# Performance work log

Measured on AMD Instinct MI355X. Metric: run time of the kernel, lower is better.

The kernel has to match this reference:

```python
import jax, jax.numpy as jnp
import numpy as np


def setup_inputs() -> dict:
    key = jax.random.key(0)
    k1, k2, k3 = jax.random.split(key, 3)
    N, M, D, K = 8192, 8192, 512, 128
    x = jax.random.normal(k1, (N, D), dtype=jnp.float32)
    target = jax.random.normal(k2, (M, D), dtype=jnp.float32)
    W = jax.random.normal(k3, (D, K), dtype=jnp.float32) * 0.05
    return {"x": x, "target": target, "W": W}


def reference(x, target, W):
    # phi_Brenier(x): convex potential f(x) = logsumexp(x @ W)  -> [N]
    phi_b = jax.nn.logsumexp(x @ W, axis=-1)
    # phi_Kantorovich = 0.5||x||^2 - phi_Brenier  -> [N]
    x_sq = jnp.sum(x * x, axis=-1)
    phi_k = 0.5 * x_sq - phi_b
    t_sq = jnp.sum(target * target, axis=-1)
    DD = 0.5 * (x_sq[:, None] + t_sq[None, :] - 2.0 * (x @ target.T))
    # C-transform: min over source points  -> [M]
    phi_c = jnp.min(DD - phi_k[:, None], axis=0)
    # Kantorovich dual objective (scalar)
    return jnp.mean(phi_k) + jnp.mean(phi_c)
```

## Files before the change

kernel.cpp:

```cpp
#include <hip/hip_runtime.h>
#include <hip/hip_bf16.h>
#include <stdint.h>

typedef __attribute__((ext_vector_type(8))) short short8;
typedef __attribute__((ext_vector_type(4))) float f32x4;
typedef __attribute__((ext_vector_type(16))) float f32x16;
typedef __attribute__((ext_vector_type(4))) int i32x4;
typedef __attribute__((ext_vector_type(8))) int i32x8;

#define N_PTS 8192
#define M_PTS 8192
#define DIM   512
#define KDIM  128

__device__ __forceinline__ unsigned fenc(float f) {
  unsigned u = __float_as_uint(f);
  return (u & 0x80000000u) ? ~u : (u | 0x80000000u);
}
__device__ __forceinline__ float fdec(unsigned k) {
  unsigned u = (k & 0x80000000u) ? (k ^ 0x80000000u) : ~k;
  return __uint_as_float(u);
}

__device__ __forceinline__ unsigned short f2bf(float f) {
  union { __hip_bfloat16 h; unsigned short u; } c;
  c.h = __float2bfloat16(f);
  return c.u;
}

__device__ __forceinline__ unsigned f2e4m3(float f) {
  unsigned u = __float_as_uint(f);
  unsigned s = (u >> 24) & 0x80;
  unsigned mag = u & 0x7fffffffu;
  unsigned r = mag + 0x0007ffffu + ((mag >> 20) & 1u);
  int e = (int)(r >> 23) - 127;
  if (e < -6) return s;
  unsigned m = (r >> 20) & 7u;
  return s | (unsigned)((e + 7) << 3) | m;
}

__device__ __forceinline__ void async_copy16(const void* g, void* l) {
  __builtin_amdgcn_global_load_lds(
      (const __attribute__((address_space(1))) void*)g,
      (__attribute__((address_space(3))) void*)l, 16, 0, 0);
}

__device__ __forceinline__ int swz_slot(int row, int slot) {
  return slot ^ ((row >> 1) & 3);
}

__device__ __forceinline__ int chunk_key(int row) {
  return ((row >> 1) & 3) ^ ((row >> 3) & 1) ^ (((row >> 4) & 1) << 1);
}

#define BARRIER __builtin_amdgcn_s_barrier()

__global__ __launch_bounds__(256)
void prep_all_kernel(const float* __restrict__ x, const float* __restrict__ tgt,
                     const float* __restrict__ W,
                     unsigned short* __restrict__ Xb, unsigned char* __restrict__ Xf8,
                     unsigned char* __restrict__ TfT, unsigned short* __restrict__ WbT,
                     float* __restrict__ xsq, float* __restrict__ tsq,
                     unsigned* __restrict__ keys) {
  const int bid = blockIdx.x;
  const int tid = threadIdx.x;
  if (bid >= (N_PTS + M_PTS) / 4) {
    const int o = (bid - (N_PTS + M_PTS) / 4) * 256 + tid;
    const int k = o >> 9, d = o & 511;
    WbT[o] = f2bf(W[d * KDIM + k]);
    return;
  }
  const int gw = (bid * 256 + tid) >> 6;
  const int j = tid & 63;
  float s;
  if (gw < N_PTS) {
    const float* src = x + (size_t)gw * DIM + j * 8;
    float4 v0 = *(const float4*)src;
    float4 v1 = *(const float4*)(src + 4);
    s = v0.x * v0.x + v0.y * v0.y + v0.z * v0.z + v0.w * v0.w +
        v1.x * v1.x + v1.y * v1.y + v1.z * v1.z + v1.w * v1.w;
    unsigned short* db = Xb + (size_t)gw * DIM + j * 8;
    ushort4 ob0, ob1;
    ob0.x = f2bf(v0.x); ob0.y = f2bf(v0.y); ob0.z = f2bf(v0.z); ob0.w = f2bf(v0.w);
    ob1.x = f2bf(v1.x); ob1.y = f2bf(v1.y); ob1.z = f2bf(v1.z); ob1.w = f2bf(v1.w);
    *(ushort4*)db = ob0;
    *(ushort4*)(db + 4) = ob1;
    unsigned long long p = (unsigned long long)f2e4m3(v0.x)
        | ((unsigned long long)f2e4m3(v0.y) << 8)
        | ((unsigned long long)f2e4m3(v0.z) << 16)
        | ((unsigned long long)f2e4m3(v0.w) << 24)
        | ((unsigned long long)f2e4m3(v1.x) << 32)
        | ((unsigned long long)f2e4m3(v1.y) << 40)
        | ((unsigned long long)f2e4m3(v1.z) << 48)
        | ((unsigned long long)f2e4m3(v1.w) << 56);
    *(unsigned long long*)(Xf8 + (size_t)gw * DIM + j * 8) = p;
#pragma unroll
    for (int m = 1; m <= 32; m <<= 1) s += __shfl_xor(s, m);
    if (j == 0) xsq[gw] = s;
  } else {
    const int tr = gw - N_PTS;
    const float* src = tgt + (size_t)tr * DIM + j * 8;
    float4 v0 = *(const float4*)src;
    float4 v1 = *(const float4*)(src + 4);
    s = v0.x * v0.x + v0.y * v0.y + v0.z * v0.z + v0.w * v0.w +
        v1.x * v1.x + v1.y * v1.y + v1.z * v1.z + v1.w * v1.w;
    unsigned long long p = (unsigned long long)f2e4m3(v0.x)
        | ((unsigned long long)f2e4m3(v0.y) << 8)
        | ((unsigned long long)f2e4m3(v0.z) << 16)
        | ((unsigned long long)f2e4m3(v0.w) << 24)
        | ((unsigned long long)f2e4m3(v1.x) << 32)
        | ((unsigned long long)f2e4m3(v1.y) << 40)
        | ((unsigned long long)f2e4m3(v1.z) << 48)
        | ((unsigned long long)f2e4m3(v1.w) << 56);
    *(unsigned long long*)(TfT + ((size_t)(j >> 3) * M_PTS + tr) * 64 + (j & 7) * 8) = p;
#pragma unroll
    for (int m = 1; m <= 32; m <<= 1) s += __shfl_xor(s, m);
    if (j == 0) { tsq[tr] = s; keys[tr] = 0xFFFFFFFFu; }
  }
}

__global__ __launch_bounds__(256)
void phi_b_kernel(const short* __restrict__ Xb, const short* __restrict__ WbT,
                  float* __restrict__ phi_b) {
  __shared__ __align__(16) short As[32 * 32];
  __shared__ __align__(16) short Bs[128 * 32];
  __shared__ __align__(16) float lg[32][136];

  const int tid = threadIdx.x;
  const int wave = tid >> 6, lane = tid & 63;
  const int n0 = blockIdx.x * 32;
  const int fr = lane & 15, g = lane >> 4;
  const int wc = wave;

  const int srow = tid >> 2;
  const int sk8 = swz_slot(srow, tid & 3) * 8;
  const int ra = tid >> 2;
  const int ska = swz_slot(ra, tid & 3) * 8;

  f32x4 acc[2][2] = {};
  for (int kt = 0; kt < 16; ++kt) {
    const int k0 = kt * 32;
    if (wave < 2)
      async_copy16(Xb + (size_t)(n0 + ra) * DIM + k0 + ska, &As[wave * 512]);
    async_copy16(WbT + (size_t)srow * DIM + k0 + sk8, &Bs[wave * 512]);
    async_copy16(WbT + (size_t)(srow + 64) * DIM + k0 + sk8, &Bs[2048 + wave * 512]);
    __syncthreads();
    short8 a[2], b[2];
#pragma unroll
    for (int i = 0; i < 2; ++i) {
      const int R = i * 16 + fr;
      a[i] = *(const short8*)&As[R * 32 + swz_slot(R, g) * 8];
    }
#pragma unroll
    for (int jx = 0; jx < 2; ++jx) {
      const int R = wc * 32 + jx * 16 + fr;
      b[jx] = *(const short8*)&Bs[R * 32 + swz_slot(R, g) * 8];
    }
#pragma unroll
    for (int i = 0; i < 2; ++i)
#pragma unroll
      for (int jx = 0; jx < 2; ++jx)
        acc[i][jx] = __builtin_amdgcn_mfma_f32_16x16x32_bf16(a[i], b[jx], acc[i][jx], 0, 0, 0);
    __syncthreads();
  }

  const int rq = g * 4;
#pragma unroll
  for (int i = 0; i < 2; ++i)
#pragma unroll
    for (int jx = 0; jx < 2; ++jx)
#pragma unroll
      for (int q = 0; q < 4; ++q)
        lg[i * 16 + rq + q][wc * 32 + jx * 16 + fr] = acc[i][jx][q];
  __syncthreads();

  const int row = tid >> 3, c8 = tid & 7;
  const float4* lr = (const float4*)(&lg[row][c8 * 16]);
  float mx = -3.4e38f;
#pragma unroll
  for (int c = 0; c < 4; ++c) {
    float4 v = lr[c];
    mx = fmaxf(mx, fmaxf(fmaxf(v.x, v.y), fmaxf(v.z, v.w)));
  }
  mx = fmaxf(mx, __shfl_xor(mx, 1));
  mx = fmaxf(mx, __shfl_xor(mx, 2));
  mx = fmaxf(mx, __shfl_xor(mx, 4));
  float s = 0.f;
#pragma unroll
  for (int c = 0; c < 4; ++c) {
    float4 v = lr[c];
    s += __expf(v.x - mx) + __expf(v.y - mx) + __expf(v.z - mx) + __expf(v.w - mx);
  }
  s += __shfl_xor(s, 1);
  s += __shfl_xor(s, 2);
  s += __shfl_xor(s, 4);
  if (c8 == 0) phi_b[n0 + row] = mx + logf(s);
}

__device__ __forceinline__ void stgA(const unsigned char* __restrict__ mat,
                                     int rowbase, int kbyte,
                                     unsigned char* dst, int tid) {
  const int r = tid >> 2, d = tid & 3;
  async_copy16(mat + (size_t)(rowbase + r) * DIM + kbyte + ((d ^ chunk_key(r)) << 4),
               dst + (tid >> 6) * 1024);
}

__device__ __forceinline__ i32x8 ld2x16(const unsigned char* p0, const unsigned char* p1) {
  i32x4 lo = *(const i32x4*)p0;
  i32x4 hi = *(const i32x4*)p1;
  return __builtin_shufflevector(lo, hi, 0, 1, 2, 3, 4, 5, 6, 7);
}

__device__ __forceinline__ f32x16 mfma_mx(i32x8 a, i32x8 b, f32x16 c) {
  return __builtin_amdgcn_mfma_scale_f32_32x32x64_f8f6f4(a, b, c, 0, 0,
                                                         0, 0x7F, 0, 0x7F);
}

template <int VMC, bool STG, bool LDB, bool BAR>
__device__ __forceinline__ void ktile(const unsigned char* Abuf, unsigned char* Sbuf,
                                      const unsigned char* __restrict__ Xf,
                                      const unsigned char* __restrict__ Bnx,
                                      int n0, int kstage, int tid, int aoff,
                                      i32x8 (&fb)[2], i32x8 (&fbn)[2],
                                      f32x16 (&acc)[4][2]) {
  i32x8 fa[4];
#pragma unroll
  for (int i = 0; i < 4; ++i)
    fa[i] = ld2x16(Abuf + aoff + i * 2048, Abuf + ((aoff + i * 2048) ^ 16));
  if (LDB) {
    fbn[0] = ld2x16(Bnx, Bnx + 16);
    fbn[1] = ld2x16(Bnx + 2048, Bnx + 2048 + 16);
  }
  if (STG) {
    stgA(Xf, n0, kstage, Sbuf, tid);
    stgA(Xf, n0 + 128, kstage, Sbuf + 8192, tid);
  }
  __builtin_amdgcn_s_setprio(1);
#pragma unroll
  for (int i = 0; i < 4; ++i) acc[i][0] = mfma_mx(fa[i], fb[0], acc[i][0]);
#pragma unroll
  for (int i = 0; i < 4; ++i) acc[i][1] = mfma_mx(fa[i], fb[1], acc[i][1]);
  __builtin_amdgcn_s_setprio(0);
  if (VMC == 6) asm volatile("s_waitcnt vmcnt(6)" ::: "memory");
  else if (VMC == 4) asm volatile("s_waitcnt vmcnt(4)" ::: "memory");
  else if (VMC == 0) asm volatile("s_waitcnt vmcnt(0)" ::: "memory");
  if (BAR) BARRIER;
}

__global__ __launch_bounds__(512, 2)
void gemm_min_kernel(const unsigned char* __restrict__ Xf, const unsigned char* __restrict__ TfT,
                     const float* __restrict__ phi_b, unsigned* __restrict__ keys) {
  __shared__ __align__(16) unsigned char lds8[49152];

  const int tid = threadIdx.x;
  const int wave = tid >> 6, lane = tid & 63;
  const int wm = wave >> 2, wn = wave & 3;
  const int fr5 = lane & 31, h = lane >> 5;

  const int bid = blockIdx.x;
  const int xcd = bid & 7, idx = bid >> 3;
  const int nt = (xcd >> 1) * 8 + (idx >> 4);
  const int mt = (xcd & 1) * 16 + (idx & 15);
  const int n0 = nt * 256, m0 = mt * 256;

  const int aoff = (wm * 128 + fr5) * 64 + (((h << 1) ^ chunk_key(fr5)) << 4);

  const unsigned char* Bb = TfT + ((size_t)(m0 + wn * 64 + fr5)) * 64 + h * 32;
#define BK_T(kt) (Bb + (size_t)(kt) * (M_PTS * 64))

  unsigned char* B0 = lds8;
  unsigned char* B1 = lds8 + 16384;
  unsigned char* B2 = lds8 + 32768;

  stgA(Xf, n0, 0, B0, tid);       stgA(Xf, n0 + 128, 0, B0 + 8192, tid);
  stgA(Xf, n0, 64, B1, tid);      stgA(Xf, n0 + 128, 64, B1 + 8192, tid);
  asm volatile("s_waitcnt vmcnt(0)" ::: "memory");
  BARRIER;

  i32x8 fbA[2], fbB[2];
  fbA[0] = ld2x16(BK_T(0), BK_T(0) + 16);
  fbA[1] = ld2x16(BK_T(0) + 2048, BK_T(0) + 2048 + 16);

  f32x16 acc[4][2] = {};
  ktile<6, true, true, true>(B0, B2, Xf, BK_T(1), n0, 128, tid, aoff, fbA, fbB, acc);
  ktile<6, true, true, true>(B1, B0, Xf, BK_T(2), n0, 192, tid, aoff, fbB, fbA, acc);
  ktile<6, true, true, true>(B2, B1, Xf, BK_T(3), n0, 256, tid, aoff, fbA, fbB, acc);
  ktile<6, true, true, true>(B0, B2, Xf, BK_T(4), n0, 320, tid, aoff, fbB, fbA, acc);
  ktile<6, true, true, true>(B1, B0, Xf, BK_T(5), n0, 384, tid, aoff, fbA, fbB, acc);
  ktile<6, true, true, true>(B2, B1, Xf, BK_T(6), n0, 448, tid, aoff, fbB, fbA, acc);
  ktile<4, false, true, true>(B0, B2, Xf, BK_T(7), n0, 0, tid, aoff, fbA, fbB, acc);
  ktile<-1, false, false, false>(B1, B2, Xf, BK_T(7), n0, 0, tid, aoff, fbB, fbA, acc);

  float mv0 = 3.4e38f, mv1 = 3.4e38f;
#pragma unroll
  for (int i = 0; i < 4; ++i) {
    float pb[16];
#pragma unroll
    for (int q = 0; q < 16; ++q)
      pb[q] = phi_b[n0 + wm * 128 + i * 32 + (q & 3) + 8 * (q >> 2) + 4 * h];
#pragma unroll
    for (int q = 0; q < 16; ++q) {
      mv0 = fminf(mv0, pb[q] - acc[i][0][q]);
      mv1 = fminf(mv1, pb[q] - acc[i][1][q]);
    }
  }
  mv0 = fminf(mv0, __shfl_xor(mv0, 32));
  mv1 = fminf(mv1, __shfl_xor(mv1, 32));
  if (h == 0) {
    atomicMin(&keys[m0 + wn * 64 + fr5], fenc(mv0));
    atomicMin(&keys[m0 + wn * 64 + 32 + fr5], fenc(mv1));
  }
#undef BK_T
}

__global__ __launch_bounds__(256)
void partial_kernel(const float* __restrict__ xsq, const float* __restrict__ phi_b,
                    const float* __restrict__ tsq, const unsigned* __restrict__ keys,
                    double* __restrict__ partials) {
  const int b = blockIdx.x, t = threadIdx.x;
  double s;
  if (b < 32) {
    const int n = b * 256 + t;
    s = 0.5 * (double)xsq[n] - (double)phi_b[n];
  } else {
    const int m = (b - 32) * 256 + t;
    s = 0.5 * (double)tsq[m] + (double)fdec(keys[m]);
  }
  const int lane = t & 63, wv = t >> 6;
#pragma unroll
  for (int k = 1; k <= 32; k <<= 1) s += __shfl_xor(s, k);
  __shared__ double ps[4];
  if (lane == 0) ps[wv] = s;
  __syncthreads();
  if (t == 0) partials[b] = ps[0] + ps[1] + ps[2] + ps[3];
}

__global__ __launch_bounds__(64)
void final_kernel(const double* __restrict__ partials, float* __restrict__ out) {
  if (threadIdx.x == 0) {
    double a = 0.0, c = 0.0;
#pragma unroll
    for (int i = 0; i < 32; ++i) a += partials[i];
#pragma unroll
    for (int i = 32; i < 64; ++i) c += partials[i];
    out[0] = (float)(a / N_PTS + c / M_PTS);
  }
}

extern "C" void kernel_launch(void* const* d_in, const int* in_sizes, int n_in,
                              void* d_out, int out_size, void* d_ws, size_t ws_size,
                              hipStream_t stream) {
  const float* x = (const float*)d_in[0];
  const float* tgt = (const float*)d_in[1];
  const float* W = (const float*)d_in[2];

  char* ws = (char*)d_ws;
  const size_t XB_BYTES = (size_t)N_PTS * DIM * 2;
  const size_t XF_BYTES = (size_t)N_PTS * DIM;
  const size_t TF_BYTES = (size_t)M_PTS * DIM;
  const size_t WT_BYTES = (size_t)KDIM * DIM * 2;
  unsigned short* Xb = (unsigned short*)ws;
  unsigned char* Xf8 = (unsigned char*)(ws + XB_BYTES);
  unsigned char* TfT = (unsigned char*)(ws + XB_BYTES + XF_BYTES);
  unsigned short* WbT = (unsigned short*)(ws + XB_BYTES + XF_BYTES + TF_BYTES);
  float* phi_b = (float*)(ws + XB_BYTES + XF_BYTES + TF_BYTES + WT_BYTES);
  float* xsq = phi_b + N_PTS;
  float* tsq = xsq + N_PTS;
  unsigned* keys = (unsigned*)(tsq + M_PTS);
  double* partials = (double*)(keys + M_PTS + 64);

  const int prep_blocks = (N_PTS + M_PTS) / 4 + (KDIM * DIM) / 256;
  prep_all_kernel<<<prep_blocks, 256, 0, stream>>>(x, tgt, W, Xb, Xf8, TfT, WbT,
                                                   xsq, tsq, keys);
  phi_b_kernel<<<N_PTS / 32, 256, 0, stream>>>((const short*)Xb, (const short*)WbT, phi_b);
  gemm_min_kernel<<<(N_PTS / 256) * (M_PTS / 256), 512, 0, stream>>>(Xf8, TfT, phi_b, keys);
  partial_kernel<<<64, 256, 0, stream>>>(xsq, phi_b, tsq, keys, partials);
  final_kernel<<<1, 64, 0, stream>>>(partials, (float*)d_out);
}
```

Before: 64.53 us.

## Load both GEMM operands directly from global in K-tiled layout, dropping LDS staging

```diff
diff --git a/kernel.cpp b/kernel.cpp
--- a/kernel.cpp
+++ b/kernel.cpp
@@ -49,16 +49,10 @@
   return slot ^ ((row >> 1) & 3);
 }
 
-__device__ __forceinline__ int chunk_key(int row) {
-  return ((row >> 1) & 3) ^ ((row >> 3) & 1) ^ (((row >> 4) & 1) << 1);
-}
-
-#define BARRIER __builtin_amdgcn_s_barrier()
-
 __global__ __launch_bounds__(256)
 void prep_all_kernel(const float* __restrict__ x, const float* __restrict__ tgt,
                      const float* __restrict__ W,
-                     unsigned short* __restrict__ Xb, unsigned char* __restrict__ Xf8,
+                     unsigned short* __restrict__ Xb, unsigned char* __restrict__ XfT,
                      unsigned char* __restrict__ TfT, unsigned short* __restrict__ WbT,
                      float* __restrict__ xsq, float* __restrict__ tsq,
                      unsigned* __restrict__ keys) {
@@ -93,7 +87,7 @@
         | ((unsigned long long)f2e4m3(v1.y) << 40)
         | ((unsigned long long)f2e4m3(v1.z) << 48)
         | ((unsigned long long)f2e4m3(v1.w) << 56);
-    *(unsigned long long*)(Xf8 + (size_t)gw * DIM + j * 8) = p;
+    *(unsigned long long*)(XfT + ((size_t)(j >> 3) * N_PTS + gw) * 64 + (j & 7) * 8) = p;
 #pragma unroll
     for (int m = 1; m <= 32; m <<= 1) s += __shfl_xor(s, m);
     if (j == 0) xsq[gw] = s;
@@ -197,14 +191,6 @@
   if (c8 == 0) phi_b[n0 + row] = mx + logf(s);
 }
 
-__device__ __forceinline__ void stgA(const unsigned char* __restrict__ mat,
-                                     int rowbase, int kbyte,
-                                     unsigned char* dst, int tid) {
-  const int r = tid >> 2, d = tid & 3;
-  async_copy16(mat + (size_t)(rowbase + r) * DIM + kbyte + ((d ^ chunk_key(r)) << 4),
-               dst + (tid >> 6) * 1024);
-}
-
 __device__ __forceinline__ i32x8 ld2x16(const unsigned char* p0, const unsigned char* p1) {
   i32x4 lo = *(const i32x4*)p0;
   i32x4 hi = *(const i32x4*)p1;
@@ -216,42 +202,37 @@
                                                          0, 0x7F, 0, 0x7F);
 }
 
-template <int VMC, bool STG, bool LDB, bool BAR>
-__device__ __forceinline__ void ktile(const unsigned char* Abuf, unsigned char* Sbuf,
-                                      const unsigned char* __restrict__ Xf,
-                                      const unsigned char* __restrict__ Bnx,
-                                      int n0, int kstage, int tid, int aoff,
-                                      i32x8 (&fb)[2], i32x8 (&fbn)[2],
-                                      f32x16 (&acc)[4][2]) {
-  i32x8 fa[4];
-#pragma unroll
-  for (int i = 0; i < 4; ++i)
-    fa[i] = ld2x16(Abuf + aoff + i * 2048, Abuf + ((aoff + i * 2048) ^ 16));
-  if (LDB) {
-    fbn[0] = ld2x16(Bnx, Bnx + 16);
-    fbn[1] = ld2x16(Bnx + 2048, Bnx + 2048 + 16);
-  }
-  if (STG) {
-    stgA(Xf, n0, kstage, Sbuf, tid);
-    stgA(Xf, n0 + 128, kstage, Sbuf + 8192, tid);
-  }
+__device__ __forceinline__ void load_set(const unsigned char* __restrict__ Ab,
+                                         const unsigned char* __restrict__ Bb,
+                                         size_t koff, i32x8 (&A)[4], i32x8 (&B)[2]) {
+#pragma unroll
+  for (int i = 0; i < 4; ++i) {
+    const unsigned char* p = Ab + koff + i * 2048;
+    A[i] = ld2x16(p, p + 16);
+  }
+#pragma unroll
+  for (int jx = 0; jx < 2; ++jx) {
+    const unsigned char* p = Bb + koff + jx * 2048;
+    B[jx] = ld2x16(p, p + 16);
+  }
+}
+
+__device__ __forceinline__ void mfma_set(const i32x8 (&A)[4], const i32x8 (&B)[2],
+                                         f32x16 (&acc)[4][2]) {
   __builtin_amdgcn_s_setprio(1);
 #pragma unroll
-  for (int i = 0; i < 4; ++i) acc[i][0] = mfma_mx(fa[i], fb[0], acc[i][0]);
-#pragma unroll
-  for (int i = 0; i < 4; ++i) acc[i][1] = mfma_mx(fa[i], fb[1], acc[i][1]);
+  for (int i = 0; i < 4; ++i) acc[i][0] = mfma_mx(A[i], B[0], acc[i][0]);
+#pragma unroll
+  for (int i = 0; i < 4; ++i) acc[i][1] = mfma_mx(A[i], B[1], acc[i][1]);
   __builtin_amdgcn_s_setprio(0);
-  if (VMC == 6) asm volatile("s_waitcnt vmcnt(6)" ::: "memory");
-  else if (VMC == 4) asm volatile("s_waitcnt vmcnt(4)" ::: "memory");
-  else if (VMC == 0) asm volatile("s_waitcnt vmcnt(0)" ::: "memory");
-  if (BAR) BARRIER;
-}
+}
+
+#define VM12 asm volatile("s_waitcnt vmcnt(12)" ::: "memory")
+#define VM0  asm volatile("s_waitcnt vmcnt(0)" ::: "memory")
 
 __global__ __launch_bounds__(512, 2)
-void gemm_min_kernel(const unsigned char* __restrict__ Xf, const unsigned char* __restrict__ TfT,
+void gemm_min_kernel(const unsigned char* __restrict__ XfT, const unsigned char* __restrict__ TfT,
                      const float* __restrict__ phi_b, unsigned* __restrict__ keys) {
-  __shared__ __align__(16) unsigned char lds8[49152];
-
   const int tid = threadIdx.x;
   const int wave = tid >> 6, lane = tid & 63;
   const int wm = wave >> 2, wn = wave & 3;
@@ -263,33 +244,24 @@
   const int mt = (xcd & 1) * 16 + (idx & 15);
   const int n0 = nt * 256, m0 = mt * 256;
 
-  const int aoff = (wm * 128 + fr5) * 64 + (((h << 1) ^ chunk_key(fr5)) << 4);
-
+  const unsigned char* Ab = XfT + ((size_t)(n0 + wm * 128 + fr5)) * 64 + h * 32;
   const unsigned char* Bb = TfT + ((size_t)(m0 + wn * 64 + fr5)) * 64 + h * 32;
-#define BK_T(kt) (Bb + (size_t)(kt) * (M_PTS * 64))
-
-  unsigned char* B0 = lds8;
-  unsigned char* B1 = lds8 + 16384;
-  unsigned char* B2 = lds8 + 32768;
-
-  stgA(Xf, n0, 0, B0, tid);       stgA(Xf, n0 + 128, 0, B0 + 8192, tid);
-  stgA(Xf, n0, 64, B1, tid);      stgA(Xf, n0 + 128, 64, B1 + 8192, tid);
-  asm volatile("s_waitcnt vmcnt(0)" ::: "memory");
-  BARRIER;
-
-  i32x8 fbA[2], fbB[2];
-  fbA[0] = ld2x16(BK_T(0), BK_T(0) + 16);
-  fbA[1] = ld2x16(BK_T(0) + 2048, BK_T(0) + 2048 + 16);
+  const size_t KT = (size_t)N_PTS * 64;
+
+  i32x8 A0[4], B0[2], A1[4], B1[2];
+  load_set(Ab, Bb, 0, A0, B0);
+  load_set(Ab, Bb, KT, A1, B1);
+  VM12;
 
   f32x16 acc[4][2] = {};
-  ktile<6, true, true, true>(B0, B2, Xf, BK_T(1), n0, 128, tid, aoff, fbA, fbB, acc);
-  ktile<6, true, true, true>(B1, B0, Xf, BK_T(2), n0, 192, tid, aoff, fbB, fbA, acc);
-  ktile<6, true, true, true>(B2, B1, Xf, BK_T(3), n0, 256, tid, aoff, fbA, fbB, acc);
-  ktile<6, true, true, true>(B0, B2, Xf, BK_T(4), n0, 320, tid, aoff, fbB, fbA, acc);
-  ktile<6, true, true, true>(B1, B0, Xf, BK_T(5), n0, 384, tid, aoff, fbA, fbB, acc);
-  ktile<6, true, true, true>(B2, B1, Xf, BK_T(6), n0, 448, tid, aoff, fbB, fbA, acc);
-  ktile<4, false, true, true>(B0, B2, Xf, BK_T(7), n0, 0, tid, aoff, fbA, fbB, acc);
-  ktile<-1, false, false, false>(B1, B2, Xf, BK_T(7), n0, 0, tid, aoff, fbB, fbA, acc);
+  mfma_set(A0, B0, acc); load_set(Ab, Bb, 2 * KT, A0, B0); VM12;
+  mfma_set(A1, B1, acc); load_set(Ab, Bb, 3 * KT, A1, B1); VM12;
+  mfma_set(A0, B0, acc); load_set(Ab, Bb, 4 * KT, A0, B0); VM12;
+  mfma_set(A1, B1, acc); load_set(Ab, Bb, 5 * KT, A1, B1); VM12;
+  mfma_set(A0, B0, acc); load_set(Ab, Bb, 6 * KT, A0, B0); VM12;
+  mfma_set(A1, B1, acc); load_set(Ab, Bb, 7 * KT, A1, B1); VM12;
+  mfma_set(A0, B0, acc); VM0;
+  mfma_set(A1, B1, acc);
 
   float mv0 = 3.4e38f, mv1 = 3.4e38f;
 #pragma unroll
@@ -310,7 +282,6 @@
     atomicMin(&keys[m0 + wn * 64 + fr5], fenc(mv0));
     atomicMin(&keys[m0 + wn * 64 + 32 + fr5], fenc(mv1));
   }
-#undef BK_T
 }
 
 __global__ __launch_bounds__(256)
@@ -360,7 +331,7 @@
   const size_t TF_BYTES = (size_t)M_PTS * DIM;
   const size_t WT_BYTES = (size_t)KDIM * DIM * 2;
   unsigned short* Xb = (unsigned short*)ws;
-  unsigned char* Xf8 = (unsigned char*)(ws + XB_BYTES);
+  unsigned char* XfT = (unsigned char*)(ws + XB_BYTES);
   unsigned char* TfT = (unsigned char*)(ws + XB_BYTES + XF_BYTES);
   unsigned short* WbT = (unsigned short*)(ws + XB_BYTES + XF_BYTES + TF_BYTES);
   float* phi_b = (float*)(ws + XB_BYTES + XF_BYTES + TF_BYTES + WT_BYTES);
@@ -370,10 +341,10 @@
   double* partials = (double*)(keys + M_PTS + 64);
 
   const int prep_blocks = (N_PTS + M_PTS) / 4 + (KDIM * DIM) / 256;
-  prep_all_kernel<<<prep_blocks, 256, 0, stream>>>(x, tgt, W, Xb, Xf8, TfT, WbT,
+  prep_all_kernel<<<prep_blocks, 256, 0, stream>>>(x, tgt, W, Xb, XfT, TfT, WbT,
                                                    xsq, tsq, keys);
   phi_b_kernel<<<N_PTS / 32, 256, 0, stream>>>((const short*)Xb, (const short*)WbT, phi_b);
-  gemm_min_kernel<<<(N_PTS / 256) * (M_PTS / 256), 512, 0, stream>>>(Xf8, TfT, phi_b, keys);
+  gemm_min_kernel<<<(N_PTS / 256) * (M_PTS / 256), 512, 0, stream>>>(XfT, TfT, phi_b, keys);
   partial_kernel<<<64, 256, 0, stream>>>(xsq, phi_b, tsq, keys, partials);
   final_kernel<<<1, 64, 0, stream>>>(partials, (float*)d_out);
 }
```

Measured after the change: 79.25 us. +22.8%, slower.
